# Optimization experiments

Measured on AMD Instinct MI355X. Metric: run time of the kernel, lower is better.

## Reference

```python
import jax, jax.numpy as jnp
import numpy as np

B, LQ, LKV = 8, 512, 512
D, H, DH, FF = 1024, 16, 64, 4096
CH, CHID = 16, 32  # AttentionBiasMLP channels
EPS_LOG = 1e-6
EPS_LN = 1e-6


def _ln(x, g, b):
    mu = jnp.mean(x, axis=-1, keepdims=True)
    var = jnp.var(x, axis=-1, keepdims=True)
    return (x - mu) * jax.lax.rsqrt(var + EPS_LN) * g + b


def setup_inputs() -> dict:
    key = jax.random.key(0)
    ks = jax.random.split(key, 24)
    s = 0.02
    inp = {
        "q": jax.random.normal(ks[0], (B, LQ, D), jnp.float32),
        "kv": jax.random.normal(ks[1], (B, LKV, D), jnp.float32),
        "attn_map": jax.random.uniform(ks[2], (B, CH, LQ + 1, LKV + 1), jnp.float32),
        # attention projections (torch Linear: y = x @ W.T + b)
        "Wq": jax.random.normal(ks[3], (D, D)) * s, "bq": jnp.zeros((D,)),
        "Wk": jax.random.normal(ks[4], (D, D)) * s, "bk": jnp.zeros((D,)),
        "Wv": jax.random.normal(ks[5], (D, D)) * s, "bv": jnp.zeros((D,)),
        "Wm": jax.random.normal(ks[6], (D, D)) * s, "bm": jnp.zeros((D,)),
        # AttentionBiasMLP 1x1 convs: weight [out_ch, in_ch]
        "Wc1": jax.random.normal(ks[7], (CHID, CH)) * s, "bc1": jnp.zeros((CHID,)),
        "Wc2": jax.random.normal(ks[8], (CH, CHID)) * s, "bc2": jnp.zeros((CH,)),
        # FFN: Linear(D,FF) -> ReLU -> Linear(FF,D)
        "Wf1": jax.random.normal(ks[9], (FF, D)) * s, "bf1": jnp.zeros((FF,)),
        "Wf2": jax.random.normal(ks[10], (D, FF)) * s, "bf2": jnp.zeros((D,)),
        # LayerNorms
        "g1": jnp.ones((D,)), "b1": jnp.zeros((D,)),
        "g2": jnp.ones((D,)), "b2": jnp.zeros((D,)),
    }
    return inp


def _forward(q, kv, attn_map, Wq, bq, Wk, bk, Wv, bv, Wm, bm,
             Wc1, bc1, Wc2, bc2, Wf1, bf1, Wf2, bf2, g1, b1, g2, b2):
    # attention bias: log of cropped attn_map through 1x1-conv MLP with exact GELU
    log_map = jnp.log(attn_map[:, :, 1:, 1:] + EPS_LOG)               # [B,CH,LQ,LKV]
    h = jnp.einsum('bcqk,oc->boqk', log_map, Wc1) + bc1[None, :, None, None]
    h = jax.nn.gelu(h, approximate=False)
    attn_bias = jnp.einsum('bcqk,oc->boqk', h, Wc2) + bc2[None, :, None, None]

    # MHAtt: project, split heads
    qh = (q @ Wq.T + bq).reshape(B, LQ, H, DH).transpose(0, 2, 1, 3)   # [B,H,LQ,DH]
    kh = (kv @ Wk.T + bk).reshape(B, LKV, H, DH).transpose(0, 2, 1, 3)
    vh = (kv @ Wv.T + bv).reshape(B, LKV, H, DH).transpose(0, 2, 1, 3)

    scores = jnp.einsum('bhqd,bhkd->bhqk', qh, kh) / np.sqrt(DH).astype(np.float32)
    scores = scores + attn_bias
    att = jax.nn.softmax(scores, axis=-1)
    ctx = jnp.einsum('bhqk,bhkd->bhqd', att, vh)                       # [B,H,LQ,DH]
    ctx = ctx.transpose(0, 2, 1, 3).reshape(B, LQ, D)
    atted = ctx @ Wm.T + bm

    x = _ln(q + atted, g1, b1)
    ffn = jax.nn.relu(x @ Wf1.T + bf1) @ Wf2.T + bf2
    x = _ln(x + ffn, g2, b2)
    return x


def reference(q, kv, attn_map, Wq, bq, Wk, bk, Wv, bv, Wm, bm,
              Wc1, bc1, Wc2, bc2, Wf1, bf1, Wf2, bf2, g1, b1, g2, b2):
    return _forward(q, kv, attn_map, Wq, bq, Wk, bk, Wv, bv, Wm, bm,
                    Wc1, bc1, Wc2, bc2, Wf1, bf1, Wf2, bf2, g1, b1, g2, b2)
```

## Files before the change

kernel.cpp:

```cpp
#include <hip/hip_runtime.h>
#include <hip/hip_bf16.h>

typedef __bf16 bf16_t;
typedef __bf16 bf16x4_t __attribute__((ext_vector_type(4)));
typedef __bf16 bf16x8_t __attribute__((ext_vector_type(8)));
typedef float  f32x4_t  __attribute__((ext_vector_type(4)));

#define B_   8
#define LQ_  512
#define LKV_ 512
#define D_   1024
#define H_   16
#define DH_  64
#define FF_  4096

__device__ __forceinline__ f32x4_t mfma16(bf16x8_t a, bf16x8_t b, f32x4_t c) {
    return __builtin_amdgcn_mfma_f32_16x16x32_bf16(a, b, c, 0, 0, 0);
}

__device__ __forceinline__ void gload_lds16(const bf16_t* g, bf16_t* l) {
    __builtin_amdgcn_global_load_lds(
        (const __attribute__((address_space(1))) void*)g,
        (__attribute__((address_space(3))) void*)l, 16, 0, 0);
}

__device__ __forceinline__ int xcd_swz(int pid, int nwg) {
    return (pid & 7) * (nwg >> 3) + (pid >> 3);
}

__device__ __forceinline__ float gelu_fast(float h) {
    const float e = exp2f(h * -2.45546696f);
    return h * __builtin_amdgcn_rcpf(1.f + e);
}

__global__ __launch_bounds__(256)
void cvt_all_kernel(const float* __restrict__ q,  const float* __restrict__ kv,
                    const float* __restrict__ Wq, const float* __restrict__ Wk,
                    const float* __restrict__ Wv, const float* __restrict__ Wm,
                    const float* __restrict__ Wf1,const float* __restrict__ Wf2,
                    const float* __restrict__ bQ, const float* __restrict__ bK,
                    const float* __restrict__ bV, float* __restrict__ bqkv,
                    bf16_t* __restrict__ dq, bf16_t* __restrict__ dW,
                    bf16_t* __restrict__ dF) {
    const int i = blockIdx.x * 256 + threadIdx.x;
    if (i >= 5242880) {
        const int j4 = i - 5242880;
        if (j4 < 768) {
            const float* s = (j4 < 256) ? bQ : (j4 < 512) ? bK : bV;
            const int jj = j4 & 255;
            ((float4*)bqkv)[j4] = ((const float4*)s)[jj];
        }
        return;
    }
    const float* s; bf16_t* d; int j;
    if (i < 1048576)      { s = q;   d = dq;           j = i; }
    else if (i < 2097152) { s = kv;  d = dq + 4194304; j = i - 1048576; }
    else if (i < 2359296) { s = Wq;  d = dW;           j = i - 2097152; }
    else if (i < 2621440) { s = Wk;  d = dW + 1048576; j = i - 2359296; }
    else if (i < 2883584) { s = Wv;  d = dW + 2097152; j = i - 2621440; }
    else if (i < 3145728) { s = Wm;  d = dW + 3145728; j = i - 2883584; }
    else if (i < 4194304) { s = Wf1; d = dF;           j = i - 3145728; }
    else                  { s = Wf2; d = dF + 4194304; j = i - 4194304; }
    const float4 v = ((const float4*)s)[j];
    bf16x4_t o;
    o[0] = (bf16_t)v.x; o[1] = (bf16_t)v.y; o[2] = (bf16_t)v.z; o[3] = (bf16_t)v.w;
    ((bf16x4_t*)d)[j] = o;
}

__global__ __launch_bounds__(256)
void bias_mlp_mfma(const float* __restrict__ amap,
                   const float* __restrict__ Wc1, const float* __restrict__ bc1,
                   const float* __restrict__ Wc2, const float* __restrict__ bc2,
                   bf16_t* __restrict__ biasb) {
    __shared__ __align__(16) char lds[4][8192];
    const int t = threadIdx.x, lane = t & 63, w = t >> 6;
    const int l15 = lane & 15, lg = lane >> 4;
    char* Xs = lds[w];
    char* Hs = lds[w] + 3072;

    bf16x8_t b1f[2], b2f;
    f32x4_t bc1v[2];
#pragma unroll
    for (int ot = 0; ot < 2; ot++) {
        bf16x8_t v;
#pragma unroll
        for (int i = 0; i < 8; i++) {
            const int kk = (lg * 8 + i) & 15;
            const float wv = Wc1[(ot * 16 + l15) * 16 + kk] * 0.69314718055994531f;
            v[i] = (lg < 2) ? (bf16_t)wv : (bf16_t)0.f;
        }
        b1f[ot] = v;
        const float bb = bc1[ot * 16 + l15];
        bc1v[ot] = f32x4_t{bb, bb, bb, bb};
    }
    {
        bf16x8_t v;
#pragma unroll
        for (int i = 0; i < 8; i++) v[i] = (bf16_t)Wc2[l15 * 32 + lg * 8 + i];
        b2f = v;
    }
    const float bc2s = bc2[l15];
    const f32x4_t cinit2 = f32x4_t{bc2s, bc2s, bc2s, bc2s};

    const int posb = (blockIdx.x * 4 + w) * 64;
    const int b  = posb >> 18;
    const int q  = (posb >> 9) & 511;
    const int k0 = posb & 511;

    const float* src = amap + (size_t)(b * 16) * 263169 + (size_t)(q + 1) * 513 + (k0 + 1 + lane);
    bf16_t xr[16];
#pragma unroll
    for (int c = 0; c < 16; c++) {
        const float v = src[(size_t)c * 263169];
        xr[c] = (bf16_t)__log2f(v + 1e-6f);
    }
    *(bf16x8_t*)(Xs + lane * 48)      = *(bf16x8_t*)&xr[0];
    *(bf16x8_t*)(Xs + lane * 48 + 16) = *(bf16x8_t*)&xr[8];

    const int lgm16 = (lg & 1) * 16;
    f32x4_t h1[4][2];
#pragma unroll
    for (int p = 0; p < 4; p++) {
        const bf16x8_t a1 = *(const bf16x8_t*)(Xs + (p * 16 + l15) * 48 + lgm16);
#pragma unroll
        for (int ot = 0; ot < 2; ot++)
            h1[p][ot] = mfma16(a1, b1f[ot], bc1v[ot]);
    }

#pragma unroll
    for (int p = 0; p < 4; p++)
#pragma unroll
        for (int ot = 0; ot < 2; ot++)
#pragma unroll
            for (int r = 0; r < 4; r++) {
                const float g = gelu_fast(h1[p][ot][r]);
                *(bf16_t*)(Hs + (p * 16 + lg * 4 + r) * 80 + (ot * 16 + l15) * 2) = (bf16_t)g;
            }

    const size_t obase = ((size_t)(b * 16 + l15) * 512 + q) * 512 + k0;
#pragma unroll
    for (int p = 0; p < 4; p++) {
        const bf16x8_t a2 = *(const bf16x8_t*)(Hs + (p * 16 + l15) * 80 + lg * 16);
        const f32x4_t o2 = mfma16(a2, b2f, cinit2);
        bf16x4_t ov;
#pragma unroll
        for (int r = 0; r < 4; r++) ov[r] = (bf16_t)o2[r];
        *(bf16x4_t*)&biasb[obase + p * 16 + lg * 4] = ov;
    }
}

template <int EPI, bool SPLIT>
__global__ __launch_bounds__(256)
void gemm_bt(const bf16_t* __restrict__ A, const bf16_t* __restrict__ A2,
             const bf16_t* __restrict__ Bw,
             const float* __restrict__ bias,
             bf16_t* __restrict__ Cb, int M, int N, int Klen, int lda) {
    __shared__ __align__(16) bf16_t As[3][128 * 32];
    __shared__ __align__(16) bf16_t Bs[3][128 * 32];
    const int t = threadIdx.x, lane = t & 63, w = t >> 6;
    const int wr = w >> 1, wc = w & 1;
    const int ntn = N >> 7;
    const int nwg = (M >> 7) * ntn;
    const int wg  = xcd_swz((int)blockIdx.x, nwg);
    const int gsz = 8 * ntn;
    const int gid = wg / gsz;
    const int rem = wg - gid * gsz;
    const int tm  = gid * 8 + (rem & 7);
    const int tn  = rem >> 3;
    const int l15 = lane & 15, lg = lane >> 4;
    const int ks = SPLIT ? blockIdx.y : 0;
    const int koff = SPLIT ? ks * Klen : 0;

    const int r0 = t >> 2,          sk0 = (t & 3) ^ ((t >> 2) & 3);
    const int r1 = (t + 256) >> 2,  sk1 = (t & 3) ^ ((t >> 2) & 3);
    const int b0 = (w * 64) * 8;
    const int b1 = (256 + w * 64) * 8;
    const bf16_t* Abase0 = A  + (size_t)(tm * 128 + r0) * lda + koff + sk0 * 8;
    const bf16_t* Abase1 = A  + (size_t)(tm * 128 + r1) * lda + koff + sk1 * 8;
    const bf16_t* Bbase0 = Bw + (size_t)(tn * 128 + r0) * lda + koff + sk0 * 8;
    const bf16_t* Bbase1 = Bw + (size_t)(tn * 128 + r1) * lda + koff + sk1 * 8;

    f32x4_t acc[4][4];
#pragma unroll
    for (int i = 0; i < 4; i++)
#pragma unroll
        for (int j = 0; j < 4; j++) acc[i][j] = f32x4_t{0.f, 0.f, 0.f, 0.f};

    const int nk = Klen >> 5;

#define STAGE128(KT, S)                                 \
    do {                                                \
        const int _ko = (KT) * 32;                      \
        gload_lds16(Abase0 + _ko, &As[(S)][b0]);        \
        gload_lds16(Abase1 + _ko, &As[(S)][b1]);        \
        gload_lds16(Bbase0 + _ko, &Bs[(S)][b0]);        \
        gload_lds16(Bbase1 + _ko, &Bs[(S)][b1]);        \
    } while (0)

    STAGE128(0, 0);
    STAGE128(1, 1);

    const int rsw = l15 & 3;
    int cur = 0;
    for (int kt = 0; kt < nk; ++kt) {
        if (kt + 1 < nk) { asm volatile("s_waitcnt vmcnt(4)" ::: "memory"); }
        else             { asm volatile("s_waitcnt vmcnt(0)" ::: "memory"); }
        __syncthreads();
        if (kt + 2 < nk) {
            const int s2 = cur >= 1 ? cur - 1 : cur + 2;
            STAGE128(kt + 2, s2);
        }

        const bf16_t* Ac = As[cur];
        const bf16_t* Bc = Bs[cur];
        bf16x8_t af[4], bfv[4];
#pragma unroll
        for (int mt = 0; mt < 4; mt++)
            af[mt] = *(const bf16x8_t*)&Ac[(wr * 64 + mt * 16 + l15) * 32 + ((lg ^ rsw) * 8)];
#pragma unroll
        for (int nt = 0; nt < 4; nt++)
            bfv[nt] = *(const bf16x8_t*)&Bc[(wc * 64 + nt * 16 + l15) * 32 + ((lg ^ rsw) * 8)];
#pragma unroll
        for (int mt = 0; mt < 4; mt++)
#pragma unroll
            for (int nt = 0; nt < 4; nt++)
                acc[mt][nt] = mfma16(af[mt], bfv[nt], acc[mt][nt]);

        cur = cur < 2 ? cur + 1 : 0;
    }
#undef STAGE128

#pragma unroll
    for (int nt = 0; nt < 4; nt++) {
        const int col = tn * 128 + wc * 64 + nt * 16 + l15;
        float bv = bias[col];
        if (SPLIT && ks != 0) bv = 0.f;
#pragma unroll
        for (int mt = 0; mt < 4; mt++) {
#pragma unroll
            for (int r = 0; r < 4; r++) {
                const int row = tm * 128 + wr * 64 + mt * 16 + lg * 4 + r;
                float v = acc[mt][nt][r] + bv;
                if (EPI == 2) v = fmaxf(v, 0.f);
                if (SPLIT)
                    Cb[(size_t)ks * M * N + (size_t)row * N + col] = (bf16_t)v;
                else Cb[(size_t)row * N + col] = (bf16_t)v;
            }
        }
    }
}

template <int EPI, bool SPLIT>
__global__ __launch_bounds__(512, 1)
void gemm8p(const bf16_t* __restrict__ A, const bf16_t* __restrict__ A2,
            const bf16_t* __restrict__ Bw, const float* __restrict__ bias,
            bf16_t* __restrict__ Cb, int M, int N, int Klen, int lda) {
    __shared__ __align__(16) bf16_t As[2][256 * 64];
    __shared__ __align__(16) bf16_t Bs[2][256 * 64];
    const int t = threadIdx.x, lane = t & 63, w = t >> 6;
    const int wr = w >> 2, wc = w & 3;
    const int l15 = lane & 15, lg = lane >> 4;
    const int ntn = N >> 8;
    const int nwg = (M >> 8) * ntn;
    const int wg  = xcd_swz((int)blockIdx.x, nwg);
    const int gsz = 8 * ntn;
    const int gid = wg / gsz;
    const int rem = wg - gid * gsz;
    const int tm  = gid * 8 + (rem & 7);
    const int tn  = rem >> 3;
    const int ks   = SPLIT ? blockIdx.y : 0;
    const int koff = SPLIT ? ks * Klen : 0;
    if (EPI == 3 && tn >= 4) A = A2;

    const int srow = w * 8 + (lane >> 3);
    const int scol = ((lane & 7) ^ (lane >> 3)) * 8;
    const bf16_t* Ag = A  + (size_t)(tm * 256 + srow) * lda + koff + scol;
    const bf16_t* Bg = Bw + (size_t)(tn * 256 + srow) * lda + koff + scol;
    const int ldsb = w * 512;

#define STAGE256(KT, S)                                                      \
    do {                                                                     \
        const size_t _ko = (size_t)(KT) * 64;                                \
        _Pragma("unroll")                                                    \
        for (int _i = 0; _i < 4; _i++) {                                     \
            gload_lds16(Ag + (size_t)(_i * 64) * lda + _ko,                  \
                        &As[(S)][_i * 4096 + ldsb]);                         \
            gload_lds16(Bg + (size_t)(_i * 64) * lda + _ko,                  \
                        &Bs[(S)][_i * 4096 + ldsb]);                         \
        }                                                                    \
    } while (0)

    f32x4_t acc[8][4];
#pragma unroll
    for (int i = 0; i < 8; i++)
#pragma unroll
        for (int j = 0; j < 4; j++) acc[i][j] = f32x4_t{0.f, 0.f, 0.f, 0.f};

    const int nk = Klen >> 6;

    STAGE256(0, 0);
    STAGE256(1, 1);

    const int rsw = l15 & 7;
    for (int kt = 0; kt < nk; ++kt) {
        const int s = kt & 1;
        if (kt + 1 < nk) { asm volatile("s_waitcnt vmcnt(8)" ::: "memory"); }
        else             { asm volatile("s_waitcnt vmcnt(0)" ::: "memory"); }
        __builtin_amdgcn_s_barrier();
        __builtin_amdgcn_sched_barrier(0);

#pragma unroll
        for (int q = 0; q < 4; q++) {
            const int mh = q >> 1, nh = q & 1;
            bf16x8_t af[4][2], bfv[2][2];
#pragma unroll
            for (int mi = 0; mi < 4; mi++) {
                const int row = wr * 128 + (mh * 4 + mi) * 16 + l15;
#pragma unroll
                for (int kk = 0; kk < 2; kk++)
                    af[mi][kk] = *(const bf16x8_t*)&As[s][row * 64 + (((kk * 4 + lg) ^ rsw) * 8)];
            }
#pragma unroll
            for (int ni = 0; ni < 2; ni++) {
                const int row = wc * 64 + (nh * 2 + ni) * 16 + l15;
#pragma unroll
                for (int kk = 0; kk < 2; kk++)
                    bfv[ni][kk] = *(const bf16x8_t*)&Bs[s][row * 64 + (((kk * 4 + lg) ^ rsw) * 8)];
            }
            __builtin_amdgcn_s_setprio(1);
#pragma unroll
            for (int mi = 0; mi < 4; mi++)
#pragma unroll
                for (int ni = 0; ni < 2; ni++)
#pragma unroll
                    for (int kk = 0; kk < 2; kk++)
                        acc[mh * 4 + mi][nh * 2 + ni] =
                            mfma16(af[mi][kk], bfv[ni][kk], acc[mh * 4 + mi][nh * 2 + ni]);
            __builtin_amdgcn_s_setprio(0);
        }

        __builtin_amdgcn_sched_barrier(0);
        __builtin_amdgcn_s_barrier();
        __builtin_amdgcn_sched_barrier(0);
        if (kt + 2 < nk) STAGE256(kt + 2, s);
    }
#undef STAGE256

#pragma unroll
    for (int n = 0; n < 4; n++) {
        const int col = tn * 256 + wc * 64 + n * 16 + l15;
        float bv = bias[col];
        if (SPLIT && ks != 0) bv = 0.f;
#pragma unroll
        for (int m = 0; m < 8; m++) {
#pragma unroll
            for (int r = 0; r < 4; r++) {
                const int row = tm * 256 + wr * 128 + m * 16 + lg * 4 + r;
                float v = acc[m][n][r] + bv;
                if (EPI == 2) v = fmaxf(v, 0.f);
                if (EPI == 3 && tn < 4) v *= 0.125f;
                if (SPLIT)
                    Cb[(size_t)ks * M * N + (size_t)row * N + col] = (bf16_t)v;
                else if (EPI == 3)
                    Cb[(size_t)(col >> 10) * 4194304 + (size_t)row * 1024 + (col & 1023)] = (bf16_t)v;
                else
                    Cb[(size_t)row * N + col] = (bf16_t)v;
            }
        }
    }
}

__global__ __launch_bounds__(256)
void attn_kernel(const bf16_t* __restrict__ Qp, const bf16_t* __restrict__ Kp,
                 const bf16_t* __restrict__ Vp, const bf16_t* __restrict__ biasb,
                 bf16_t* __restrict__ ctx) {
    __shared__ __align__(16) bf16_t Qs[64 * 64];
    __shared__ __align__(16) bf16_t Ks[64 * 64];
    __shared__ __align__(16) bf16_t Vts[64 * 64];
    __shared__ __align__(16) bf16_t Ps[64 * 64];
    __shared__ __align__(16) bf16_t Bbs[64 * 64];

    const int bid = xcd_swz((int)blockIdx.x, 1024);
    const int qt = bid & 7, h = (bid >> 3) & 15, b = bid >> 7;
    const int t = threadIdx.x, lane = t & 63, w = t >> 6;
    const int l15 = lane & 15, lg = lane >> 4;

#pragma unroll
    for (int i = 0; i < 2; i++) {
        const int c = t + i * 256;
        const int row = c >> 3, cg = c & 7;
        const uint4 v = *(const uint4*)&Qp[(((size_t)(b * LQ_ + qt * 64 + row)) * H_ + h) * DH_ + cg * 8];
        *(uint4*)((char*)Qs + row * 128 + ((cg ^ (row & 7)) << 4)) = v;
    }
    __syncthreads();

    bf16x8_t aq[2];
    {
        const int rowq = w * 16 + l15;
#pragma unroll
        for (int kc = 0; kc < 2; kc++)
            aq[kc] = *(const bf16x8_t*)((const char*)Qs + rowq * 128 + (((kc * 4 + lg) ^ (rowq & 7)) << 4));
    }

    f32x4_t oacc[4];
#pragma unroll
    for (int i = 0; i < 4; i++) oacc[i] = f32x4_t{0.f, 0.f, 0.f, 0.f};
    float mrow[4] = {-1e30f, -1e30f, -1e30f, -1e30f};
    float lrow[4] = {0.f, 0.f, 0.f, 0.f};

    const bf16_t* bias_tile = biasb + ((size_t)(b * H_ + h) * LQ_ + qt * 64) * LKV_;

    for (int kt = 0; kt < 8; ++kt) {
        __syncthreads();
#pragma unroll
        for (int i = 0; i < 2; i++) {
            const int c = t + i * 256;
            const int row = c >> 3, cg = c & 7;
            const uint4 v = *(const uint4*)&Kp[(((size_t)(b * LKV_ + kt * 64 + row)) * H_ + h) * DH_ + cg * 8];
            *(uint4*)((char*)Ks + row * 128 + ((cg ^ (row & 7)) << 4)) = v;
        }
#pragma unroll
        for (int i = 0; i < 2; i++) {
            const int c = t + i * 256;
            const int row = c >> 3, cg = c & 7;
            const uint4 bv4 = *(const uint4*)&bias_tile[(size_t)row * LKV_ + kt * 64 + cg * 8];
            *(uint4*)&Bbs[row * 64 + cg * 8] = bv4;
        }
#pragma unroll
        for (int i = 0; i < 2; i++) {
            const int c = t + i * 256;
            const int k = c >> 3, dg = c & 7;
            const bf16x8_t vv = *(const bf16x8_t*)&Vp[(((size_t)(b * LKV_ + kt * 64 + k)) * H_ + h) * DH_ + dg * 8];
#pragma unroll
            for (int j = 0; j < 8; j++) {
                const int d = dg * 8 + j;
                *(bf16_t*)((char*)Vts + d * 128 + ((((k * 2) >> 4) ^ (d & 7)) << 4) + ((k * 2) & 15)) = vv[j];
            }
        }
        __syncthreads();

        f32x4_t sacc[4];
#pragma unroll
        for (int i = 0; i < 4; i++) sacc[i] = f32x4_t{0.f, 0.f, 0.f, 0.f};
#pragma unroll
        for (int nt = 0; nt < 4; nt++) {
            const int rowk = nt * 16 + l15;
#pragma unroll
            for (int kc = 0; kc < 2; kc++) {
                const bf16x8_t bk = *(const bf16x8_t*)((const char*)Ks + rowk * 128 + (((kc * 4 + lg) ^ (rowk & 7)) << 4));
                sacc[nt] = mfma16(aq[kc], bk, sacc[nt]);
            }
        }

        float esc[4];
#pragma unroll
        for (int r = 0; r < 4; r++) {
            const int qr = w * 16 + lg * 4 + r;
            float mx = -1e30f;
#pragma unroll
            for (int nt = 0; nt < 4; nt++) {
                const float bvv = (float)Bbs[qr * 64 + nt * 16 + l15];
                const float v = sacc[nt][r] + bvv;
                sacc[nt][r] = v;
                mx = fmaxf(mx, v);
            }
#pragma unroll
            for (int msk = 8; msk >= 1; msk >>= 1) mx = fmaxf(mx, __shfl_xor(mx, msk));
            const float mnew = fmaxf(mrow[r], mx);
            esc[r] = __expf(mrow[r] - mnew);
            mrow[r] = mnew;
            float rs = 0.f;
#pragma unroll
            for (int nt = 0; nt < 4; nt++) {
                const float p = __expf(sacc[nt][r] - mnew);
                sacc[nt][r] = p;
                rs += p;
            }
#pragma unroll
            for (int msk = 8; msk >= 1; msk >>= 1) rs += __shfl_xor(rs, msk);
            lrow[r] = lrow[r] * esc[r] + rs;
        }

#pragma unroll
        for (int r = 0; r < 4; r++) {
            const int prow = w * 16 + lg * 4 + r;
#pragma unroll
            for (int nt = 0; nt < 4; nt++) {
                const int pc2 = (nt * 16 + l15) * 2;
                *(bf16_t*)((char*)Ps + prow * 128 + (((pc2 >> 4) ^ (prow & 7)) << 4) + (pc2 & 15)) =
                    (bf16_t)sacc[nt][r];
            }
        }
        asm volatile("s_waitcnt lgkmcnt(0)" ::: "memory");
        __builtin_amdgcn_sched_barrier(0);

#pragma unroll
        for (int dt = 0; dt < 4; dt++)
#pragma unroll
            for (int r = 0; r < 4; r++) oacc[dt][r] *= esc[r];

        bf16x8_t pa[2];
        {
            const int rowp = w * 16 + l15;
#pragma unroll
            for (int kc = 0; kc < 2; kc++)
                pa[kc] = *(const bf16x8_t*)((const char*)Ps + rowp * 128 + (((kc * 4 + lg) ^ (rowp & 7)) << 4));
        }
#pragma unroll
        for (int dt = 0; dt < 4; dt++) {
            const int rowv = dt * 16 + l15;
#pragma unroll
            for (int kc = 0; kc < 2; kc++) {
                const bf16x8_t bv = *(const bf16x8_t*)((const char*)Vts + rowv * 128 + (((kc * 4 + lg) ^ (rowv & 7)) << 4));
                oacc[dt] = mfma16(pa[kc], bv, oacc[dt]);
            }
        }
    }

    float inv[4];
#pragma unroll
    for (int r = 0; r < 4; r++) inv[r] = __builtin_amdgcn_rcpf(lrow[r]);
#pragma unroll
    for (int dt = 0; dt < 4; dt++) {
#pragma unroll
        for (int r = 0; r < 4; r++) {
            const float v = oacc[dt][r] * inv[r];
            const int q = qt * 64 + w * 16 + lg * 4 + r;
            const int d = dt * 16 + l15;
            ctx[(((size_t)(b * LQ_ + q)) * H_ + h) * DH_ + d] = (bf16_t)v;
        }
    }
}

__global__ __launch_bounds__(256)
void add_ln3_mid_kernel(const bf16_t* __restrict__ Xb, const bf16_t* __restrict__ Y0,
                        const bf16_t* __restrict__ Y1,
                        const float* __restrict__ g, const float* __restrict__ be,
                        bf16_t* __restrict__ ob) {
    const int row = blockIdx.x, t = threadIdx.x;
    const bf16x4_t xv = ((const bf16x4_t*)(Xb + (size_t)row * 1024))[t];
    const bf16x4_t y0 = ((const bf16x4_t*)(Y0 + (size_t)row * 1024))[t];
    const bf16x4_t y1 = ((const bf16x4_t*)(Y1 + (size_t)row * 1024))[t];
    float v[4];
#pragma unroll
    for (int i = 0; i < 4; i++)
        v[i] = (float)xv[i] + (float)y0[i] + (float)y1[i];
    float s = v[0] + v[1] + v[2] + v[3];
    float s2 = v[0] * v[0] + v[1] * v[1] + v[2] * v[2] + v[3] * v[3];
#pragma unroll
    for (int m = 32; m >= 1; m >>= 1) { s += __shfl_xor(s, m); s2 += __shfl_xor(s2, m); }
    __shared__ float red[8];
    const int w = t >> 6, lane = t & 63;
    if (lane == 0) { red[w] = s; red[4 + w] = s2; }
    __syncthreads();
    s = red[0] + red[1] + red[2] + red[3];
    s2 = red[4] + red[5] + red[6] + red[7];
    const float mu = s * (1.f / 1024.f);
    const float var = s2 * (1.f / 1024.f) - mu * mu;
    const float rstd = rsqrtf(var + 1e-6f);
    const float4 gv = ((const float4*)g)[t];
    const float4 bv = ((const float4*)be)[t];
    bf16x4_t qo;
    qo[0] = (bf16_t)((v[0] - mu) * rstd * gv.x + bv.x);
    qo[1] = (bf16_t)((v[1] - mu) * rstd * gv.y + bv.y);
    qo[2] = (bf16_t)((v[2] - mu) * rstd * gv.z + bv.z);
    qo[3] = (bf16_t)((v[3] - mu) * rstd * gv.w + bv.w);
    ((bf16x4_t*)(ob + (size_t)row * 1024))[t] = qo;
}

__global__ __launch_bounds__(256)
void add_ln5_fin_kernel(const bf16_t* __restrict__ Xb, const bf16_t* __restrict__ Y0,
                        const bf16_t* __restrict__ Y1, const bf16_t* __restrict__ Y2,
                        const bf16_t* __restrict__ Y3,
                        const float* __restrict__ g, const float* __restrict__ be,
                        float* __restrict__ of) {
    const int row = blockIdx.x, t = threadIdx.x;
    const bf16x4_t xv = ((const bf16x4_t*)(Xb + (size_t)row * 1024))[t];
    const bf16x4_t y0 = ((const bf16x4_t*)(Y0 + (size_t)row * 1024))[t];
    const bf16x4_t y1 = ((const bf16x4_t*)(Y1 + (size_t)row * 1024))[t];
    const bf16x4_t y2 = ((const bf16x4_t*)(Y2 + (size_t)row * 1024))[t];
    const bf16x4_t y3 = ((const bf16x4_t*)(Y3 + (size_t)row * 1024))[t];
    float v[4];
#pragma unroll
    for (int i = 0; i < 4; i++)
        v[i] = (float)xv[i] + ((float)y0[i] + (float)y1[i]) + ((float)y2[i] + (float)y3[i]);
    float s = v[0] + v[1] + v[2] + v[3];
    float s2 = v[0] * v[0] + v[1] * v[1] + v[2] * v[2] + v[3] * v[3];
#pragma unroll
    for (int m = 32; m >= 1; m >>= 1) { s += __shfl_xor(s, m); s2 += __shfl_xor(s2, m); }
    __shared__ float red[8];
    const int w = t >> 6, lane = t & 63;
    if (lane == 0) { red[w] = s; red[4 + w] = s2; }
    __syncthreads();
    s = red[0] + red[1] + red[2] + red[3];
    s2 = red[4] + red[5] + red[6] + red[7];
    const float mu = s * (1.f / 1024.f);
    const float var = s2 * (1.f / 1024.f) - mu * mu;
    const float rstd = rsqrtf(var + 1e-6f);
    const float4 gv = ((const float4*)g)[t];
    const float4 bv = ((const float4*)be)[t];
    float o[4];
    o[0] = (v[0] - mu) * rstd * gv.x + bv.x;
    o[1] = (v[1] - mu) * rstd * gv.y + bv.y;
    o[2] = (v[2] - mu) * rstd * gv.z + bv.z;
    o[3] = (v[3] - mu) * rstd * gv.w + bv.w;
    ((float4*)(of + (size_t)row * 1024))[t] = make_float4(o[0], o[1], o[2], o[3]);
}

extern "C" void kernel_launch(void* const* d_in, const int* in_sizes, int n_in,
                              void* d_out, int out_size, void* d_ws, size_t ws_size,
                              hipStream_t stream) {
    (void)in_sizes; (void)n_in; (void)out_size; (void)ws_size;
    const float* q    = (const float*)d_in[0];
    const float* kv   = (const float*)d_in[1];
    const float* amap = (const float*)d_in[2];
    const float* Wq = (const float*)d_in[3];  const float* bQ = (const float*)d_in[4];
    const float* Wk = (const float*)d_in[5];  const float* bK = (const float*)d_in[6];
    const float* Wv = (const float*)d_in[7];  const float* bV = (const float*)d_in[8];
    const float* Wm = (const float*)d_in[9];  const float* bM = (const float*)d_in[10];
    const float* Wc1 = (const float*)d_in[11]; const float* bc1 = (const float*)d_in[12];
    const float* Wc2 = (const float*)d_in[13]; const float* bc2 = (const float*)d_in[14];
    const float* Wf1 = (const float*)d_in[15]; const float* bf1 = (const float*)d_in[16];
    const float* Wf2 = (const float*)d_in[17]; const float* bf2 = (const float*)d_in[18];
    const float* g1 = (const float*)d_in[19]; const float* b1 = (const float*)d_in[20];
    const float* g2 = (const float*)d_in[21]; const float* b2 = (const float*)d_in[22];

    char* w = (char*)d_ws;
    bf16_t* biasb = (bf16_t*)(w);
    bf16_t* p0    = (bf16_t*)(w);
    bf16_t* p1    = (bf16_t*)(w + 8388608);
    bf16_t* hb    = (bf16_t*)(w);
    bf16_t* f0    = (bf16_t*)(w + 33554432);
    bf16_t* qb   = (bf16_t*)(w + 67108864);
    bf16_t* kvb  = (bf16_t*)(w + 75497472);
    bf16_t* Qp   = (bf16_t*)(w + 83886080);
    bf16_t* Kp   = (bf16_t*)(w + 92274688);
    bf16_t* Vp   = (bf16_t*)(w + 100663296);
    bf16_t* Wqkvb = (bf16_t*)(w + 109051904);
    bf16_t* Wmb  = (bf16_t*)(w + 115343360);
    bf16_t* Wf1b = (bf16_t*)(w + 117440512);
    bf16_t* Wf2b = (bf16_t*)(w + 125829120);
    float*  bqkv = (float*)(w + 134217728);
    bf16_t* ctx  = (bf16_t*)(w + 150994944);
    bf16_t* xb  = Vp;

    dim3 blk(256);
    cvt_all_kernel<<<20483, blk, 0, stream>>>(q, kv, Wq, Wk, Wv, Wm, Wf1, Wf2,
                                              bQ, bK, bV, bqkv, qb, Wqkvb, Wf1b);

    bias_mlp_mfma<<<8192, blk, 0, stream>>>(amap, Wc1, bc1, Wc2, bc2, biasb);

    gemm8p<3, false><<<192, dim3(512), 0, stream>>>(qb, kvb, Wqkvb, bqkv, Qp,
                                                    4096, 3072, 1024, 1024);

    attn_kernel<<<1024, blk, 0, stream>>>(Qp, Kp, Vp, biasb, ctx);

    gemm_bt<0, true><<<dim3(256, 2), blk, 0, stream>>>(ctx, nullptr, Wmb, bM, p0,
                                                       4096, 1024, 512, 1024);
    add_ln3_mid_kernel<<<4096, blk, 0, stream>>>(qb, p0, p1, g1, b1, xb);

    gemm8p<2, false><<<256, dim3(512), 0, stream>>>(xb, nullptr, Wf1b, bf1, hb,
                                                    4096, 4096, 1024, 1024);
    gemm8p<0, true><<<dim3(64, 4), dim3(512), 0, stream>>>(hb, nullptr, Wf2b, bf2, f0,
                                                           4096, 1024, 1024, 4096);
    add_ln5_fin_kernel<<<4096, blk, 0, stream>>>(xb, f0, f0 + 4194304, f0 + 8388608,
                                                 f0 + 12582912, g2, b2, (float*)d_out);
}
```

Before: 312.0 us.

## Merge bias MLP and QKV projection into one interleaved heterogeneous kernel

```diff
diff --git a/kernel.cpp b/kernel.cpp
--- a/kernel.cpp
+++ b/kernel.cpp
@@ -67,16 +67,16 @@
     ((bf16x4_t*)d)[j] = o;
 }
 
-__global__ __launch_bounds__(256)
-void bias_mlp_mfma(const float* __restrict__ amap,
-                   const float* __restrict__ Wc1, const float* __restrict__ bc1,
-                   const float* __restrict__ Wc2, const float* __restrict__ bc2,
-                   bf16_t* __restrict__ biasb) {
-    __shared__ __align__(16) char lds[4][8192];
+__device__ __forceinline__
+void bias_body(char* ldsall, int bbid,
+               const float* __restrict__ amap,
+               const float* __restrict__ Wc1, const float* __restrict__ bc1,
+               const float* __restrict__ Wc2, const float* __restrict__ bc2,
+               bf16_t* __restrict__ biasb) {
     const int t = threadIdx.x, lane = t & 63, w = t >> 6;
     const int l15 = lane & 15, lg = lane >> 4;
-    char* Xs = lds[w];
-    char* Hs = lds[w] + 3072;
+    char* Xs = ldsall + w * 8192;
+    char* Hs = Xs + 3072;
 
     bf16x8_t b1f[2], b2f;
     f32x4_t bc1v[2];
@@ -102,7 +102,7 @@
     const float bc2s = bc2[l15];
     const f32x4_t cinit2 = f32x4_t{bc2s, bc2s, bc2s, bc2s};
 
-    const int posb = (blockIdx.x * 4 + w) * 64;
+    const int posb = (bbid * 4 + w) * 64;
     const int b  = posb >> 18;
     const int q  = (posb >> 9) & 511;
     const int k0 = posb & 511;
@@ -147,6 +147,116 @@
         for (int r = 0; r < 4; r++) ov[r] = (bf16_t)o2[r];
         *(bf16x4_t*)&biasb[obase + p * 16 + lg * 4] = ov;
     }
+}
+
+__device__ __forceinline__
+void qkv_body(char* ldsall, int pid,
+              const bf16_t* __restrict__ Aq, const bf16_t* __restrict__ Akv,
+              const bf16_t* __restrict__ Bw, const float* __restrict__ bias,
+              bf16_t* __restrict__ Cb) {
+    bf16_t* As = (bf16_t*)ldsall;
+    bf16_t* Bs = (bf16_t*)(ldsall + 24576);
+    const int t = threadIdx.x, lane = t & 63, w = t >> 6;
+    const int wr = w >> 1, wc = w & 1;
+    const int ntn = 24;
+    const int gsz = 8 * ntn;
+    const int gid = pid / gsz;
+    const int rem = pid - gid * gsz;
+    const int tm  = gid * 8 + (rem & 7);
+    const int tn  = rem >> 3;
+    const int l15 = lane & 15, lg = lane >> 4;
+    const int lda = 1024;
+    const bf16_t* A = (tn >= 8) ? Akv : Aq;
+
+    const int r0 = t >> 2,          sk0 = (t & 3) ^ ((t >> 2) & 3);
+    const int r1 = (t + 256) >> 2;
+    const int b0 = (w * 64) * 8;
+    const int b1 = (256 + w * 64) * 8;
+    const bf16_t* Abase0 = A  + (size_t)(tm * 128 + r0) * lda + sk0 * 8;
+    const bf16_t* Abase1 = A  + (size_t)(tm * 128 + r1) * lda + sk0 * 8;
+    const bf16_t* Bbase0 = Bw + (size_t)(tn * 128 + r0) * lda + sk0 * 8;
+    const bf16_t* Bbase1 = Bw + (size_t)(tn * 128 + r1) * lda + sk0 * 8;
+
+    f32x4_t acc[4][4];
+#pragma unroll
+    for (int i = 0; i < 4; i++)
+#pragma unroll
+        for (int j = 0; j < 4; j++) acc[i][j] = f32x4_t{0.f, 0.f, 0.f, 0.f};
+
+    const int nk = 32;
+
+#define STAGEQ(KT, S)                                        \
+    do {                                                     \
+        const int _ko = (KT) * 32;                           \
+        gload_lds16(Abase0 + _ko, &As[(S) * 4096 + b0]);     \
+        gload_lds16(Abase1 + _ko, &As[(S) * 4096 + b1]);     \
+        gload_lds16(Bbase0 + _ko, &Bs[(S) * 4096 + b0]);     \
+        gload_lds16(Bbase1 + _ko, &Bs[(S) * 4096 + b1]);     \
+    } while (0)
+
+    STAGEQ(0, 0);
+    STAGEQ(1, 1);
+
+    const int rsw = l15 & 3;
+    int cur = 0;
+    for (int kt = 0; kt < nk; ++kt) {
+        if (kt + 1 < nk) { asm volatile("s_waitcnt vmcnt(4)" ::: "memory"); }
+        else             { asm volatile("s_waitcnt vmcnt(0)" ::: "memory"); }
+        __syncthreads();
+        if (kt + 2 < nk) {
+            const int s2 = cur >= 1 ? cur - 1 : cur + 2;
+            STAGEQ(kt + 2, s2);
+        }
+
+        const bf16_t* Ac = &As[cur * 4096];
+        const bf16_t* Bc = &Bs[cur * 4096];
+        bf16x8_t af[4], bfv[4];
+#pragma unroll
+        for (int mt = 0; mt < 4; mt++)
+            af[mt] = *(const bf16x8_t*)&Ac[(wr * 64 + mt * 16 + l15) * 32 + ((lg ^ rsw) * 8)];
+#pragma unroll
+        for (int nt = 0; nt < 4; nt++)
+            bfv[nt] = *(const bf16x8_t*)&Bc[(wc * 64 + nt * 16 + l15) * 32 + ((lg ^ rsw) * 8)];
+#pragma unroll
+        for (int mt = 0; mt < 4; mt++)
+#pragma unroll
+            for (int nt = 0; nt < 4; nt++)
+                acc[mt][nt] = mfma16(af[mt], bfv[nt], acc[mt][nt]);
+
+        cur = cur < 2 ? cur + 1 : 0;
+    }
+#undef STAGEQ
+
+#pragma unroll
+    for (int nt = 0; nt < 4; nt++) {
+        const int col = tn * 128 + wc * 64 + nt * 16 + l15;
+        const float bv = bias[col];
+#pragma unroll
+        for (int mt = 0; mt < 4; mt++) {
+#pragma unroll
+            for (int r = 0; r < 4; r++) {
+                const int row = tm * 128 + wr * 64 + mt * 16 + lg * 4 + r;
+                float v = acc[mt][nt][r] + bv;
+                if (tn < 8) v *= 0.125f;
+                Cb[(size_t)(col >> 10) * 4194304 + (size_t)row * 1024 + (col & 1023)] = (bf16_t)v;
+            }
+        }
+    }
+}
+
+__global__ __launch_bounds__(256)
+void bias_qkv_kernel(const float* __restrict__ amap,
+                     const float* __restrict__ Wc1, const float* __restrict__ bc1,
+                     const float* __restrict__ Wc2, const float* __restrict__ bc2,
+                     bf16_t* __restrict__ biasb,
+                     const bf16_t* __restrict__ Aq, const bf16_t* __restrict__ Akv,
+                     const bf16_t* __restrict__ Bw, const float* __restrict__ bqkv,
+                     bf16_t* __restrict__ Cb) {
+    __shared__ __align__(16) char lds[49152];
+    const int bid = blockIdx.x;
+    const int grp = bid / 35, rem = bid - grp * 35;
+    if (rem < 3) qkv_body(lds, grp * 3 + rem, Aq, Akv, Bw, bqkv, Cb);
+    else         bias_body(lds, grp * 32 + (rem - 3), amap, Wc1, bc1, Wc2, bc2, biasb);
 }
 
 template <int EPI, bool SPLIT>
@@ -172,13 +282,13 @@
     const int koff = SPLIT ? ks * Klen : 0;
 
     const int r0 = t >> 2,          sk0 = (t & 3) ^ ((t >> 2) & 3);
-    const int r1 = (t + 256) >> 2,  sk1 = (t & 3) ^ ((t >> 2) & 3);
+    const int r1 = (t + 256) >> 2;
     const int b0 = (w * 64) * 8;
     const int b1 = (256 + w * 64) * 8;
     const bf16_t* Abase0 = A  + (size_t)(tm * 128 + r0) * lda + koff + sk0 * 8;
-    const bf16_t* Abase1 = A  + (size_t)(tm * 128 + r1) * lda + koff + sk1 * 8;
+    const bf16_t* Abase1 = A  + (size_t)(tm * 128 + r1) * lda + koff + sk0 * 8;
     const bf16_t* Bbase0 = Bw + (size_t)(tn * 128 + r0) * lda + koff + sk0 * 8;
-    const bf16_t* Bbase1 = Bw + (size_t)(tn * 128 + r1) * lda + koff + sk1 * 8;
+    const bf16_t* Bbase1 = Bw + (size_t)(tn * 128 + r1) * lda + koff + sk0 * 8;
 
     f32x4_t acc[4][4];
 #pragma unroll
@@ -270,7 +380,6 @@
     const int tn  = rem >> 3;
     const int ks   = SPLIT ? blockIdx.y : 0;
     const int koff = SPLIT ? ks * Klen : 0;
-    if (EPI == 3 && tn >= 4) A = A2;
 
     const int srow = w * 8 + (lane >> 3);
     const int scol = ((lane & 7) ^ (lane >> 3)) * 8;
@@ -358,11 +467,8 @@
                 const int row = tm * 256 + wr * 128 + m * 16 + lg * 4 + r;
                 float v = acc[m][n][r] + bv;
                 if (EPI == 2) v = fmaxf(v, 0.f);
-                if (EPI == 3 && tn < 4) v *= 0.125f;
                 if (SPLIT)
                     Cb[(size_t)ks * M * N + (size_t)row * N + col] = (bf16_t)v;
-                else if (EPI == 3)
-                    Cb[(size_t)(col >> 10) * 4194304 + (size_t)row * 1024 + (col & 1023)] = (bf16_t)v;
                 else
                     Cb[(size_t)row * N + col] = (bf16_t)v;
             }
@@ -648,10 +754,8 @@
     cvt_all_kernel<<<20483, blk, 0, stream>>>(q, kv, Wq, Wk, Wv, Wm, Wf1, Wf2,
                                               bQ, bK, bV, bqkv, qb, Wqkvb, Wf1b);
 
-    bias_mlp_mfma<<<8192, blk, 0, stream>>>(amap, Wc1, bc1, Wc2, bc2, biasb);
-
-    gemm8p<3, false><<<192, dim3(512), 0, stream>>>(qb, kvb, Wqkvb, bqkv, Qp,
-                                                    4096, 3072, 1024, 1024);
+    bias_qkv_kernel<<<8960, blk, 0, stream>>>(amap, Wc1, bc1, Wc2, bc2, biasb,
+                                              qb, kvb, Wqkvb, bqkv, Qp);
 
     attn_kernel<<<1024, blk, 0, stream>>>(Qp, Kp, Vp, biasb, ctx);
 
```

Result: no change. 312.2 us (+0.1%).
